# Kernel optimization log

Hardware: AMD Instinct MI355X
Metric: run time of the kernel (lower is better)

Reference implementation:

```python
import jax, jax.numpy as jnp
import numpy as np

B, T, D, H = 64, 256, 1024, 1024


def setup_inputs() -> dict:
    key = jax.random.key(0)
    ks = jax.random.split(key, 7)
    s = 0.02
    x = jax.random.normal(ks[0], (B, T, D), dtype=jnp.float32)
    # packed gate weights, gate order [i, f, g, o] along last dim (4H)
    Wx0 = jax.random.normal(ks[1], (D, 4 * H), dtype=jnp.float32) * s
    Wh0 = jax.random.normal(ks[2], (H, 4 * H), dtype=jnp.float32) * s
    b0 = jnp.zeros((4 * H,), dtype=jnp.float32)
    Wx1 = jax.random.normal(ks[3], (H, 4 * H), dtype=jnp.float32) * s
    Wh1 = jax.random.normal(ks[4], (H, 4 * H), dtype=jnp.float32) * s
    b1 = jnp.zeros((4 * H,), dtype=jnp.float32)
    return {"x": x, "Wx0": Wx0, "Wh0": Wh0, "b0": b0, "Wx1": Wx1, "Wh1": Wh1, "b1": b1}


def _cell(h, c, xt, Wx, Wh, b):
    gates = xt @ Wx + h @ Wh + b  # [B, 4H]
    i, f, g, o = jnp.split(gates, 4, axis=-1)
    c_new = jax.nn.sigmoid(f) * c + jax.nn.sigmoid(i) * jnp.tanh(g)
    h_new = jax.nn.sigmoid(o) * jnp.tanh(c_new)
    return h_new, c_new


def reference(x, Wx0, Wh0, b0, Wx1, Wh1, b1):
    b = x.shape[0]
    h = x.dtype
    z = jnp.zeros((b, Wh0.shape[0]), dtype=x.dtype)
    carry0 = (z, z, z, z)  # (h0, c0, h1, c1), zero-initialized like flax initialize_carry

    def step(carry, xt):
        h0, c0, h1, c1 = carry
        h0, c0 = _cell(h0, c0, xt, Wx0, Wh0, b0)
        h1, c1 = _cell(h1, c1, h0, Wx1, Wh1, b1)
        return (h0, c0, h1, c1), None

    xs = jnp.swapaxes(x, 0, 1)  # [T, B, D]
    (h0, c0, h1, c1), _ = jax.lax.scan(step, carry0, xs)
    return h1  # last-timestep output of top layer, [B, H]
```

## Files before the change

### kernel.cpp

```cpp
#include <hip/hip_runtime.h>
#include <cmath>

#define TSTEPS 256
#define DIM 1024

typedef _Float16 half8v __attribute__((ext_vector_type(8)));
typedef _Float16 half4v __attribute__((ext_vector_type(4)));
typedef float f32x4 __attribute__((ext_vector_type(4)));
typedef unsigned long long u64;


__global__ void prologue(const float* __restrict__ x, _Float16* __restrict__ xh,
                         _Float16* __restrict__ hrings, unsigned* __restrict__ cnts)
{
    size_t gid  = (size_t)blockIdx.x * blockDim.x + threadIdx.x;
    size_t nthr = (size_t)gridDim.x * blockDim.x;
    for (size_t i = gid; i < 4194304u; i += nthr) {
        float4 v = ((const float4*)x)[i];
        half4v h = {(_Float16)v.x, (_Float16)v.y, (_Float16)v.z, (_Float16)v.w};
        unsigned d4 = (unsigned)i & 255u, t = ((unsigned)i >> 8) & 255u, b = (unsigned)i >> 16;
        ((half4v*)(xh + ((size_t)t * 64 + b) * 1024))[d4] = h;
    }
    for (size_t i = gid; i < 65536u; i += nthr) {
        half8v z = {};
        ((half8v*)hrings)[i] = z;
    }
    for (size_t i = gid; i < 139264u; i += nthr) cnts[i] = 0u;
}

__global__ __launch_bounds__(512, 2)
void lstm_persistent(const float* __restrict__ Wx0, const float* __restrict__ Wh0,
                     const float* __restrict__ b0,
                     const float* __restrict__ Wx1, const float* __restrict__ Wh1,
                     const float* __restrict__ b1,
                     const _Float16* __restrict__ xh, _Float16* __restrict__ h0r,
                     _Float16* __restrict__ h1r, unsigned* __restrict__ cnts,
                     float* __restrict__ out)
{
    extern __shared__ char smem[];
    _Float16* wfrag = (_Float16*)smem;
    float*    gates = (float*)smem;

    const int tid  = threadIdx.x;
    const int blk  = blockIdx.x;
    const int cell = blk >> 7;
    const int wb   = blk & 127;
    const int mb   = wb >> 6, nb = wb & 63;
    const int lane = tid & 63, kq = tid >> 6;
    const int n15 = lane & 15, q = lane >> 4;

    unsigned* leaf0 = cnts;
    unsigned* leaf1 = cnts + 65536;
    unsigned* leafm = cell ? leaf1 : leaf0;

    half8v wreg[32];
    {
        const float* passW[2] = { cell ? Wx1 : Wx0, cell ? Wh1 : Wh0 };
        for (int ps = 0; ps < 2; ++ps) {
            const float* W = passW[ps];
            for (int idx = tid; idx < 16384; idx += 512) {
                int k = idx >> 4;
                int cc0 = (idx & 15) * 4;
                const float* src = W + (size_t)k * 4096
                                   + (cc0 >> 4) * 1024 + nb * 16 + (cc0 & 15);
                float4 v = *(const float4*)src;
                int skq = k >> 8, kt = (k >> 5) & 7, qp = (k >> 3) & 3, j = k & 7;
                float vv[4] = {v.x, v.y, v.z, v.w};
                #pragma unroll
                for (int e = 0; e < 4; ++e) {
                    int cc = cc0 + e, nt = cc >> 4, nn = cc & 15;
                    wfrag[((((skq * 4 + nt) * 8 + kt) * 64) + qp * 16 + nn) * 8 + j]
                        = (_Float16)vv[e];
                }
            }
            __syncthreads();
            if ((kq >> 2) == ps) {
                int skq = kq & 3;
                #pragma unroll
                for (int nt = 0; nt < 4; ++nt)
                    #pragma unroll
                    for (int kt = 0; kt < 8; ++kt)
                        wreg[nt * 8 + kt] = *(const half8v*)
                            &wfrag[((((skq * 4 + nt) * 8 + kt) * 64) + lane) * 8];
            }
            __syncthreads();
        }
    }

    const int pm = tid >> 4, pdn = tid & 15;
    const float* bias = cell ? b1 : b0;
    const int dimg = nb * 16 + pdn;
    const float bi = bias[0 * 1024 + dimg], bfg = bias[1 * 1024 + dimg],
                bg = bias[2 * 1024 + dimg], bo  = bias[3 * 1024 + dimg];
    float creg = 0.0f;

    const bool havex = (cell == 0) && (kq < 4);

    for (int p = 0; p <= TSTEPS; ++p) {
        if (cell == 0 && p == TSTEPS) break;
        const bool active = cell ? (p >= 1) : true;

        half8v A[2][8];
        if (havex) {
            const _Float16* a = xh + (size_t)p * 65536
                                + (size_t)(mb * 32 + n15) * 1024 + kq * 256 + q * 8;
            #pragma unroll
            for (int mt = 0; mt < 2; ++mt)
                #pragma unroll
                for (int kt = 0; kt < 8; ++kt)
                    A[mt][kt] = *(const half8v*)(a + mt * 16384 + kt * 32);
        }

        if (tid < 64) {
            if (p >= 1) {
                const unsigned* addr = nullptr;
                if (tid < 16) {
                    addr = leaf0 + ((p - 1) * 16 + tid) * 16;
                } else if (tid < 32) {
                    int lf = tid - 16;
                    if (cell == 0) { if (p >= 3) addr = leaf1 + ((p - 3) * 16 + lf) * 16; }
                    else           { if (p >= 2) addr = leaf1 + ((p - 1) * 16 + lf) * 16; }
                }
                bool ok = (addr == nullptr);
                while (true) {
                    if (!ok)
                        ok = __hip_atomic_load(addr, __ATOMIC_RELAXED,
                                               __HIP_MEMORY_SCOPE_AGENT) >= 8u;
                    if (__ballot(ok) == ~0ull) break;
                    __builtin_amdgcn_s_sleep(1);
                }
            }
            __builtin_amdgcn_fence(__ATOMIC_ACQUIRE, "agent");
        }
        __syncthreads();

        if (active && !havex) {
            const _Float16* hb; int ks;
            if (cell == 0)   { hb = h0r + (size_t)((p - 1) & 3) * 65536; ks = kq - 4; }
            else if (kq < 4) { hb = h0r + (size_t)((p - 1) & 3) * 65536; ks = kq; }
            else             { hb = h1r + (size_t)((p - 2) & 3) * 65536; ks = kq - 4; }
            const _Float16* a = hb + (size_t)mb * 32768
                                + (size_t)(ks * 16 + (q >> 1)) * 512
                                + (size_t)n15 * 16 + (q & 1) * 8;
            #pragma unroll
            for (int mt = 0; mt < 2; ++mt)
                #pragma unroll
                for (int kt = 0; kt < 8; ++kt)
                    A[mt][kt] = *(const half8v*)(a + kt * 1024 + mt * 256);
        }

        if (active) {
            #pragma unroll
            for (int mt = 0; mt < 2; ++mt) {
                f32x4 acc[4] = {{0.f,0.f,0.f,0.f}, {0.f,0.f,0.f,0.f},
                                {0.f,0.f,0.f,0.f}, {0.f,0.f,0.f,0.f}};
                #pragma unroll
                for (int kt = 0; kt < 8; ++kt)
                    #pragma unroll
                    for (int nt = 0; nt < 4; ++nt)
                        acc[nt] = __builtin_amdgcn_mfma_f32_16x16x32_f16(
                                      A[mt][kt], wreg[nt * 8 + kt], acc[nt], 0, 0, 0);
                const int row0 = mt * 16 + q * 4;
                #pragma unroll
                for (int nt = 0; nt < 4; ++nt) {
                    const int c = nt * 16 + n15;
                    *(f32x4*)(gates + (c * 8 + kq) * 32
                                    + (row0 ^ ((c & 7) << 2))) = acc[nt];
                }
            }
        }
        __syncthreads();

        if (active) {
            float gg[4];
            #pragma unroll
            for (int g = 0; g < 4; ++g) {
                const int c = g * 16 + pdn;
                const int key = (c & 7) << 2;
                float s = 0.f;
                #pragma unroll
                for (int k8 = 0; k8 < 8; ++k8)
                    s += gates[(c * 8 + k8) * 32 + (pm ^ key)];
                gg[g] = s;
            }
            float g0 = gg[0] + bi, g1 = gg[1] + bfg, g2 = gg[2] + bg, g3 = gg[3] + bo;
            float si = 1.f / (1.f + __expf(-g0));
            float sf = 1.f / (1.f + __expf(-g1));
            float so = 1.f / (1.f + __expf(-g3));
            float tg = 1.f - 2.f / (__expf(2.f * g2) + 1.f);
            float cn = sf * creg + si * tg;
            float tc = 1.f - 2.f / (__expf(2.f * cn) + 1.f);
            float hn = so * tc;
            creg = cn;
            if (p < TSTEPS) {
                union { _Float16 h; unsigned short u; } cv; cv.h = (_Float16)hn;
                _Float16* dst = (cell ? h1r + (size_t)((p - 1) & 3) * 65536
                                      : h0r + (size_t)(p & 3) * 65536)
                                + (size_t)mb * 32768 + (size_t)nb * 512;
                __hip_atomic_store((unsigned short*)dst + tid, cv.u,
                                   __ATOMIC_RELAXED, __HIP_MEMORY_SCOPE_AGENT);
            }
            if (cell && p == TSTEPS) out[(mb * 32 + pm) * 1024 + nb * 16 + pdn] = hn;
        }

        if (p < TSTEPS) {
            if (active) {
                asm volatile("s_waitcnt vmcnt(0)" ::: "memory");
                __syncthreads();
            }
            if (tid == 0)
                __hip_atomic_fetch_add(leafm + (p * 16 + (wb >> 3)) * 16, 1u,
                                       __ATOMIC_RELAXED, __HIP_MEMORY_SCOPE_AGENT);
        }
    }
}

extern "C" void kernel_launch(void* const* d_in, const int* in_sizes, int n_in,
                              void* d_out, int out_size, void* d_ws, size_t ws_size,
                              hipStream_t stream)
{
    const float* x   = (const float*)d_in[0];
    const float* Wx0 = (const float*)d_in[1];
    const float* Wh0 = (const float*)d_in[2];
    const float* b0  = (const float*)d_in[3];
    const float* Wx1 = (const float*)d_in[4];
    const float* Wh1 = (const float*)d_in[5];
    const float* b1  = (const float*)d_in[6];
    float* out = (float*)d_out;

    _Float16* xh   = (_Float16*)d_ws;
    _Float16* h0r  = xh + (size_t)16777216;
    _Float16* h1r  = h0r + 262144;
    unsigned* cnts = (unsigned*)(h1r + 262144);

    hipLaunchKernelGGL(prologue, dim3(2048), dim3(256), 0, stream, x, xh, h0r, cnts);

    size_t smem = 131072;
    (void)hipFuncSetAttribute((const void*)lstm_persistent,
                              hipFuncAttributeMaxDynamicSharedMemorySize, (int)smem);

    void* args[] = {(void*)&Wx0, (void*)&Wh0, (void*)&b0,
                    (void*)&Wx1, (void*)&Wh1, (void*)&b1,
                    (void*)&xh, (void*)&h0r, (void*)&h1r,
                    (void*)&cnts, (void*)&out};
    (void)hipLaunchCooperativeKernel((const void*)lstm_persistent, dim3(256), dim3(512),
                                     args, (unsigned)smem, stream);
}
```

Before: 1.852 ms.

## Replace block-wide step barrier with per-wave fine-grained readiness polling

Each wave now polls only the two leaf counters covering the h slice it reads, instead of the first wave polling all counters and then the whole block meeting at a barrier. Waves that only read x skip the wait before their MFMA work and poll after it, purely to keep the ring-buffer ordering safe. This removes one __syncthreads per step and lets x-fed waves overlap their matmul with waiting for other blocks. The risk is subtle ordering mistakes in the inter-block ring protocol, since each wave now does its own acquire fence.

```diff
diff --git a/kernel.cpp b/kernel.cpp
--- a/kernel.cpp
+++ b/kernel.cpp
@@ -95,6 +95,7 @@
     float creg = 0.0f;
 
     const bool havex = (cell == 0) && (kq < 4);
+    const int  ks    = (kq < 4) ? kq : kq - 4;
 
     for (int p = 0; p <= TSTEPS; ++p) {
         if (cell == 0 && p == TSTEPS) break;
@@ -109,17 +110,17 @@
                 #pragma unroll
                 for (int kt = 0; kt < 8; ++kt)
                     A[mt][kt] = *(const half8v*)(a + mt * 16384 + kt * 32);
-        }
-
-        if (tid < 64) {
-            if (p >= 1) {
+        } else {
+            {
                 const unsigned* addr = nullptr;
-                if (tid < 16) {
-                    addr = leaf0 + ((p - 1) * 16 + tid) * 16;
-                } else if (tid < 32) {
-                    int lf = tid - 16;
-                    if (cell == 0) { if (p >= 3) addr = leaf1 + ((p - 3) * 16 + lf) * 16; }
-                    else           { if (p >= 2) addr = leaf1 + ((p - 1) * 16 + lf) * 16; }
+                if (lane < 2) {
+                    if (cell == 0) {
+                        if (p >= 1) addr = leaf0 + (((p - 1) * 16 + mb * 8 + ks * 2 + lane) * 16);
+                    } else if (kq < 4) {
+                        if (p >= 1) addr = leaf0 + (((p - 1) * 16 + mb * 8 + ks * 2 + lane) * 16);
+                    } else {
+                        if (p >= 2) addr = leaf1 + (((p - 1) * 16 + mb * 8 + ks * 2 + lane) * 16);
+                    }
                 }
                 bool ok = (addr == nullptr);
                 while (true) {
@@ -129,24 +130,22 @@
                     if (__ballot(ok) == ~0ull) break;
                     __builtin_amdgcn_s_sleep(1);
                 }
-            }
-            __builtin_amdgcn_fence(__ATOMIC_ACQUIRE, "agent");
-        }
-        __syncthreads();
-
-        if (active && !havex) {
-            const _Float16* hb; int ks;
-            if (cell == 0)   { hb = h0r + (size_t)((p - 1) & 3) * 65536; ks = kq - 4; }
-            else if (kq < 4) { hb = h0r + (size_t)((p - 1) & 3) * 65536; ks = kq; }
-            else             { hb = h1r + (size_t)((p - 2) & 3) * 65536; ks = kq - 4; }
-            const _Float16* a = hb + (size_t)mb * 32768
-                                + (size_t)(ks * 16 + (q >> 1)) * 512
-                                + (size_t)n15 * 16 + (q & 1) * 8;
-            #pragma unroll
-            for (int mt = 0; mt < 2; ++mt)
-                #pragma unroll
-                for (int kt = 0; kt < 8; ++kt)
-                    A[mt][kt] = *(const half8v*)(a + kt * 1024 + mt * 256);
+                __builtin_amdgcn_fence(__ATOMIC_ACQUIRE, "agent");
+            }
+            if (active) {
+                const _Float16* hb;
+                if (cell == 0)   hb = h0r + (size_t)((p - 1) & 3) * 65536;
+                else if (kq < 4) hb = h0r + (size_t)((p - 1) & 3) * 65536;
+                else             hb = h1r + (size_t)((p - 2) & 3) * 65536;
+                const _Float16* a = hb + (size_t)mb * 32768
+                                    + (size_t)(ks * 16 + (q >> 1)) * 512
+                                    + (size_t)n15 * 16 + (q & 1) * 8;
+                #pragma unroll
+                for (int mt = 0; mt < 2; ++mt)
+                    #pragma unroll
+                    for (int kt = 0; kt < 8; ++kt)
+                        A[mt][kt] = *(const half8v*)(a + kt * 1024 + mt * 256);
+            }
         }
 
         if (active) {
@@ -167,6 +166,23 @@
                     *(f32x4*)(gates + (c * 8 + kq) * 32
                                     + (row0 ^ ((c & 7) << 2))) = acc[nt];
                 }
+            }
+        }
+
+        if (havex) {
+            const unsigned* addr = nullptr;
+            if (lane < 2) {
+                if (p >= 1) addr = leaf0 + (((p - 1) * 16 + mb * 8 + ks * 2 + lane) * 16);
+            } else if (lane < 4) {
+                if (p >= 3) addr = leaf1 + (((p - 3) * 16 + mb * 8 + ks * 2 + (lane - 2)) * 16);
+            }
+            bool ok = (addr == nullptr);
+            while (true) {
+                if (!ok)
+                    ok = __hip_atomic_load(addr, __ATOMIC_RELAXED,
+                                           __HIP_MEMORY_SCOPE_AGENT) >= 8u;
+                if (__ballot(ok) == ~0ull) break;
+                __builtin_amdgcn_s_sleep(1);
             }
         }
         __syncthreads();
```

Measured after the change: 4.321 ms. +133.2%, slower.
